# Kernel tuning notes

Hardware: AMD Instinct MI355X
Metric: run time of the kernel (lower is better)

The kernel has to match this reference:

```python
import jax, jax.numpy as jnp
import numpy as np

N_LAYERS = 4
NEG_SLOPE = 0.2  # GATv2 leaky_relu slope


def _segment_softmax(alpha, seg, num):
    # alpha: [E, H], seg: [E] target-node ids; every node has a self loop so no empty segments
    amax = jax.ops.segment_max(alpha, seg, num_segments=num)
    a = jnp.exp(alpha - amax[seg])
    denom = jax.ops.segment_sum(a, seg, num_segments=num)
    return a / denom[seg]


def _gat_block(x, relations, src, dst, rel_idx, Wl, bl, Wr, br, We, att, bias, Wb, bb):
    N, D = x.shape
    H = att.shape[0]
    C = att.shape[1]

    edge_attr = relations[rel_idx]  # [E, D]
    # add_self_loops with fill_value='mean': self-loop edge_attr = mean of incoming edge attrs
    deg = jax.ops.segment_sum(jnp.ones_like(dst, dtype=x.dtype), dst, num_segments=N)
    loop_attr = jax.ops.segment_sum(edge_attr, dst, num_segments=N) / jnp.maximum(deg, 1.0)[:, None]
    loops = jnp.arange(N, dtype=src.dtype)
    src_all = jnp.concatenate([src, loops])
    dst_all = jnp.concatenate([dst, loops])
    ea = jnp.concatenate([edge_attr, loop_attr], axis=0)  # [E+N, D]

    xl = (x @ Wl + bl).reshape(N, H, C)  # lin_l -> source transform
    xr = (x @ Wr + br).reshape(N, H, C)  # lin_r -> target transform
    eproj = (ea @ We).reshape(-1, H, C)  # lin_edge (no bias in PyG GATv2Conv)

    m = xl[src_all] + xr[dst_all] + eproj          # [E+N, H, C]
    m = jnp.where(m > 0, m, NEG_SLOPE * m)          # leaky_relu
    alpha = jnp.einsum('ehc,hc->eh', m, att)        # [E+N, H]
    alpha = _segment_softmax(alpha, dst_all, N)

    msg = xl[src_all] * alpha[..., None]            # [E+N, H, C]
    out = jax.ops.segment_sum(msg, dst_all, num_segments=N)  # [N, H, C]
    x_out = out.mean(axis=1) + bias                 # concat=False -> head mean, then bias

    # relation update: gnn.lin_edge -> relu -> block lin_edge
    r = jax.nn.relu(relations @ We)                 # [R, H*C]
    r_out = r @ Wb + bb                             # [R, D]
    return x_out, r_out


def setup_inputs() -> dict:
    key = jax.random.key(0)
    N, E, R, D, H = 10000, 40000, 2000, 128, 8
    L = N_LAYERS
    ks = jax.random.split(key, 16)
    s = 1.0 / np.sqrt(D)
    sb = 1.0 / np.sqrt(H * D)
    return {
        'x': jax.random.normal(ks[0], (N, D), dtype=jnp.float32),
        'edge_index': jax.random.randint(ks[1], (2, E), 0, N),
        'relations': jax.random.normal(ks[2], (R, D), dtype=jnp.float32),
        'relation_index': jax.random.randint(ks[3], (E,), 0, R),
        'Wl': jax.random.normal(ks[4], (L, D, H * D), dtype=jnp.float32) * s,
        'bl': jnp.zeros((L, H * D), dtype=jnp.float32),
        'Wr': jax.random.normal(ks[5], (L, D, H * D), dtype=jnp.float32) * s,
        'br': jnp.zeros((L, H * D), dtype=jnp.float32),
        'We': jax.random.normal(ks[6], (L, D, H * D), dtype=jnp.float32) * s,
        'att': jax.random.normal(ks[7], (L, H, D), dtype=jnp.float32) * s,
        'bias': jnp.zeros((L, D), dtype=jnp.float32),
        'Wb': jax.random.normal(ks[8], (L, H * D, D), dtype=jnp.float32) * sb,
        'bb': jnp.zeros((L, D), dtype=jnp.float32),
    }


def reference(x, edge_index, relations, relation_index, Wl, bl, Wr, br, We, att, bias, Wb, bb):
    src, dst = edge_index[0], edge_index[1]
    for l in range(N_LAYERS):
        x, relations = _gat_block(x, relations, src, dst, relation_index,
                                  Wl[l], bl[l], Wr[l], br[l], We[l], att[l],
                                  bias[l], Wb[l], bb[l])
    return (x, relations)
```

## Files before the change

kernel.cpp:

```cpp
#include <hip/hip_runtime.h>
#include <hip/hip_bf16.h>
#include <math.h>

#define NEG_SLOPE 0.2f
#define N_LAYERS 4

typedef __bf16 bf16_t;
typedef __attribute__((ext_vector_type(8))) __bf16 bf16x8;
typedef __attribute__((ext_vector_type(4))) __bf16 bf16x4;
typedef __attribute__((ext_vector_type(4))) float f32x4;
typedef __attribute__((ext_vector_type(8))) float f32x8;

static __device__ __forceinline__ float leaky(float v){ return v > 0.f ? v : NEG_SLOPE * v; }


__global__ void fill_int_kernel(int* __restrict__ p, int v, int n){
  int i = blockIdx.x*blockDim.x + threadIdx.x;
  if(i < n) p[i] = v;
}

__global__ void fill_bias_kernel(float* __restrict__ out, const float* __restrict__ b, int rows){
  int i = blockIdx.x*blockDim.x + threadIdx.x;
  if(i < rows * 128) out[i] = b[i & 127];
}

__global__ void hist_kernel(const int* __restrict__ dst, int E, int* __restrict__ deg){
  int e = blockIdx.x*blockDim.x + threadIdx.x;
  if(e < E) atomicAdd(&deg[dst[e]], 1);
}

__global__ void scan_kernel(const int* __restrict__ deg, int* __restrict__ offs, int N){
  __shared__ int wsum[4];
  int t = threadIdx.x, lane = t & 63, w = t >> 6;
  int carry = 0;
  for(int base = 0; base < N; base += 256){
    int v = (base + t < N) ? deg[base + t] : 0;
    int s = v;
#pragma unroll
    for(int o = 1; o < 64; o <<= 1){
      int u = __shfl_up(s, o);
      if(lane >= o) s += u;
    }
    if(lane == 63) wsum[w] = s;
    __syncthreads();
    int woff = 0;
    for(int i = 0; i < w; ++i) woff += wsum[i];
    if(base + t < N) offs[base + t + 1] = carry + woff + s;
    int tot = wsum[0] + wsum[1] + wsum[2] + wsum[3];
    __syncthreads();
    carry += tot;
  }
  if(t == 0) offs[0] = 0;
}

__global__ void scatter_kernel(const int* __restrict__ src, const int* __restrict__ dst,
                               const int* __restrict__ rel, int E,
                               const int* __restrict__ offs, int* __restrict__ cursor,
                               int* __restrict__ srcs, int* __restrict__ rels){
  int e = blockIdx.x*blockDim.x + threadIdx.x;
  if(e < E){
    int d = dst[e];
    int pos = offs[d] + atomicAdd(&cursor[d], 1);
    srcs[pos] = src[e];
    rels[pos] = rel[e];
  }
}


__global__ void deg_bhist_kernel(const int* __restrict__ offs, int N, int* __restrict__ blkhist){
  __shared__ int h[256];
  int t = threadIdx.x;
  h[t] = 0; __syncthreads();
  int i = blockIdx.x * 256 + t;
  if(i < N){
    int d = offs[i+1] - offs[i]; if(d > 255) d = 255;
    atomicAdd(&h[d], 1);
  }
  __syncthreads();
  blkhist[blockIdx.x * 256 + t] = h[t];
}

__global__ void deg_base_kernel(int* __restrict__ blkhist, int nb){
  __shared__ int tot[256];
  int d = threadIdx.x;
  int s = 0;
  for(int b = 0; b < nb; ++b){
    int v = blkhist[b * 256 + d];
    blkhist[b * 256 + d] = s;
    s += v;
  }
  tot[d] = s; __syncthreads();
  int start = 0;
  for(int k = d + 1; k < 256; ++k) start += tot[k];
  for(int b = 0; b < nb; ++b) blkhist[b * 256 + d] += start;
}

__global__ void deg_place_kernel(const int* __restrict__ offs, int N,
                                 const int* __restrict__ blkhist, int* __restrict__ order){
  __shared__ int cur[256];
  int t = threadIdx.x;
  cur[t] = blkhist[blockIdx.x * 256 + t];
  __syncthreads();
  int i = blockIdx.x * 256 + t;
  if(i < N){
    int d = offs[i+1] - offs[i]; if(d > 255) d = 255;
    int pos = atomicAdd(&cur[d], 1);
    order[pos] = i;
  }
}


__global__ void transpose_split_all_kernel(
    const float* __restrict__ Wl, const float* __restrict__ Wr,
    const float* __restrict__ We, const float* __restrict__ Wb,
    bf16_t* __restrict__ tWlh, bf16_t* __restrict__ tWll,
    bf16_t* __restrict__ tWrh, bf16_t* __restrict__ tWrl,
    bf16_t* __restrict__ tWeh, bf16_t* __restrict__ tWel,
    bf16_t* __restrict__ tWbh, bf16_t* __restrict__ tWbl){
  __shared__ float t[32][33];
  const int z = blockIdx.z, type = z >> 2, layer = z & 3;
  const int K  = (type < 3) ? 128 : 1024;
  const int Nn = (type < 3) ? 1024 : 128;
  const float* W; bf16_t* Th; bf16_t* Tl;
  if(type == 0){ W = Wl; Th = tWlh; Tl = tWll; }
  else if(type == 1){ W = Wr; Th = tWrh; Tl = tWrl; }
  else if(type == 2){ W = We; Th = tWeh; Tl = tWel; }
  else { W = Wb; Th = tWbh; Tl = tWbl; }
  size_t wo = (size_t)layer * 131072;
  W += wo; Th += wo; Tl += wo;
  const int nbx = K / 32;
  const int bx = blockIdx.x % nbx, by = blockIdx.x / nbx;
  const int k0 = bx * 32, n0 = by * 32;
  const int tx = threadIdx.x, ty = threadIdx.y;
#pragma unroll
  for(int i = 0; i < 4; ++i)
    t[ty*4 + i][tx] = W[(size_t)(k0 + ty*4 + i) * Nn + n0 + tx];
  __syncthreads();
#pragma unroll
  for(int i = 0; i < 4; ++i){
    int n = ty*4 + i;
    float v = t[tx][n];
    bf16_t h = (bf16_t)v;
    bf16_t l = (bf16_t)(v - (float)h);
    Th[(size_t)(n0 + n) * K + k0 + tx] = h;
    Tl[(size_t)(n0 + n) * K + k0 + tx] = l;
  }
}


template<bool RELU_A, bool HAS_BIAS, bool WRITE_BF16, bool SPLITK>
__global__ __launch_bounds__(256) void gemm_mfma_kernel(
    const float* __restrict__ A,
    const bf16_t* __restrict__ Bt_hi, const bf16_t* __restrict__ Bt_lo,
    const float* __restrict__ bias, float* __restrict__ C, bf16_t* __restrict__ Cb,
    int M, int N, int K){
  constexpr int LDK = 40;
  __shared__ bf16_t Ah[128 * LDK];
  __shared__ bf16_t Al[128 * LDK];
  __shared__ bf16_t Bh[128 * LDK];
  __shared__ bf16_t Bl[128 * LDK];

  const int tid  = threadIdx.x;
  const int lane = tid & 63;
  const int wid  = tid >> 6;
  const int wm = wid >> 1, wn = wid & 1;
  const int row0 = blockIdx.y * 128, col0 = blockIdx.x * 128;
  const int l15 = lane & 15;
  const int kb  = (lane >> 4) * 8;

  f32x4 acc[4][4];
#pragma unroll
  for(int m = 0; m < 4; ++m)
#pragma unroll
    for(int n = 0; n < 4; ++n) acc[m][n] = (f32x4){0.f, 0.f, 0.f, 0.f};

  int kbeg = 0, kend = K;
  if(SPLITK){ kbeg = blockIdx.z * 128; kend = kbeg + 128; }

  for(int k0 = kbeg; k0 < kend; k0 += 32){
    __syncthreads();
#pragma unroll
    for(int i = 0; i < 4; ++i){
      int f = tid + i * 256;
      int r = f >> 3, kq = f & 7;
      float4 v = make_float4(0.f, 0.f, 0.f, 0.f);
      if(row0 + r < M) v = *(const float4*)(A + (size_t)(row0 + r) * K + k0 + kq * 4);
      if(RELU_A){ v.x = fmaxf(v.x, 0.f); v.y = fmaxf(v.y, 0.f); v.z = fmaxf(v.z, 0.f); v.w = fmaxf(v.w, 0.f); }
      bf16_t h0 = (bf16_t)v.x, h1 = (bf16_t)v.y, h2 = (bf16_t)v.z, h3 = (bf16_t)v.w;
      bf16x4 hv = (bf16x4){h0, h1, h2, h3};
      bf16x4 lv = (bf16x4){(bf16_t)(v.x - (float)h0), (bf16_t)(v.y - (float)h1),
                           (bf16_t)(v.z - (float)h2), (bf16_t)(v.w - (float)h3)};
      *(bf16x4*)&Ah[r * LDK + kq * 4] = hv;
      *(bf16x4*)&Al[r * LDK + kq * 4] = lv;
    }
#pragma unroll
    for(int i = 0; i < 2; ++i){
      int f = tid + i * 256;
      int n = f >> 2, kq = f & 3;
      *(bf16x8*)&Bh[n * LDK + kq * 8] = *(const bf16x8*)(Bt_hi + (size_t)(col0 + n) * K + k0 + kq * 8);
      *(bf16x8*)&Bl[n * LDK + kq * 8] = *(const bf16x8*)(Bt_lo + (size_t)(col0 + n) * K + k0 + kq * 8);
    }
    __syncthreads();

    bf16x8 ah[4], al[4], bh[4], bl[4];
#pragma unroll
    for(int m = 0; m < 4; ++m){
      int r = wm * 64 + m * 16 + l15;
      ah[m] = *(bf16x8*)&Ah[r * LDK + kb];
      al[m] = *(bf16x8*)&Al[r * LDK + kb];
    }
#pragma unroll
    for(int n = 0; n < 4; ++n){
      int c = wn * 64 + n * 16 + l15;
      bh[n] = *(bf16x8*)&Bh[c * LDK + kb];
      bl[n] = *(bf16x8*)&Bl[c * LDK + kb];
    }
#pragma unroll
    for(int m = 0; m < 4; ++m)
#pragma unroll
      for(int n = 0; n < 4; ++n){
        acc[m][n] = __builtin_amdgcn_mfma_f32_16x16x32_bf16(ah[m], bh[n], acc[m][n], 0, 0, 0);
        acc[m][n] = __builtin_amdgcn_mfma_f32_16x16x32_bf16(ah[m], bl[n], acc[m][n], 0, 0, 0);
        acc[m][n] = __builtin_amdgcn_mfma_f32_16x16x32_bf16(al[m], bh[n], acc[m][n], 0, 0, 0);
      }
  }

#pragma unroll
  for(int n = 0; n < 4; ++n){
    int col = col0 + wn * 64 + n * 16 + l15;
    float bv = HAS_BIAS ? bias[col] : 0.f;
#pragma unroll
    for(int m = 0; m < 4; ++m){
      int rbase = row0 + wm * 64 + m * 16 + (lane >> 4) * 4;
#pragma unroll
      for(int r = 0; r < 4; ++r){
        if(rbase + r < M){
          size_t idx = (size_t)(rbase + r) * N + col;
          if(SPLITK){
            atomicAdd(&C[idx], acc[m][n][r]);
          } else {
            float val = acc[m][n][r] + bv;
            C[idx] = val;
            if(WRITE_BF16) Cb[idx] = (bf16_t)val;
          }
        }
      }
    }
  }
}


__global__ __launch_bounds__(256, 3) void gemm_proj_kernel(
    const float* __restrict__ Ar, const float* __restrict__ Ax,
    const bf16_t* __restrict__ Weh, const bf16_t* __restrict__ Wel,
    const bf16_t* __restrict__ Wlh, const bf16_t* __restrict__ Wll,
    const bf16_t* __restrict__ Wrh, const bf16_t* __restrict__ Wrl,
    const float* __restrict__ biasL, const float* __restrict__ biasR,
    float* __restrict__ rproj, bf16_t* __restrict__ rpb,
    bf16_t* __restrict__ xlb, bf16_t* __restrict__ xrb,
    int R, int Nn, int rjobs, int xjobs){
  constexpr int LDK = 40;
  __shared__ char smem[40960];
  bf16_t* Ah = (bf16_t*)smem;
  bf16_t* Al = (bf16_t*)(smem + 10240);
  bf16_t* Bh = (bf16_t*)(smem + 20480);
  bf16_t* Bl = (bf16_t*)(smem + 30720);

  const int tid  = threadIdx.x;
  const int lane = tid & 63;
  const int wid  = tid >> 6;
  const int wm = wid >> 1, wn = wid & 1;
  const int l15 = lane & 15;
  const int kb  = (lane >> 4) * 8;

  int nwg = gridDim.x;
  int lin = blockIdx.x;
  int w = ((nwg & 7) == 0) ? ((lin & 7) * (nwg >> 3) + (lin >> 3)) : lin;
  int job, jw;
  if(w < rjobs){ job = 0; jw = w; }
  else if(w < rjobs + xjobs){ job = 1; jw = w - rjobs; }
  else { job = 2; jw = w - rjobs - xjobs; }

  const float*  A   = (job == 0) ? Ar : Ax;
  const bf16_t* Bth = (job == 0) ? Weh : (job == 1) ? Wlh : Wrh;
  const bf16_t* Btl = (job == 0) ? Wel : (job == 1) ? Wll : Wrl;
  const int M = (job == 0) ? R : Nn;
  const int row0 = (jw >> 3) * 128, col0 = (jw & 7) * 128;

  f32x4 acc[4][4];
#pragma unroll
  for(int m = 0; m < 4; ++m)
#pragma unroll
    for(int n = 0; n < 4; ++n) acc[m][n] = (f32x4){0.f, 0.f, 0.f, 0.f};

  for(int k0 = 0; k0 < 128; k0 += 32){
    __syncthreads();
#pragma unroll
    for(int i = 0; i < 4; ++i){
      int f = tid + i * 256;
      int r = f >> 3, kq = f & 7;
      float4 v = make_float4(0.f, 0.f, 0.f, 0.f);
      if(row0 + r < M) v = *(const float4*)(A + (size_t)(row0 + r) * 128 + k0 + kq * 4);
      bf16_t h0 = (bf16_t)v.x, h1 = (bf16_t)v.y, h2 = (bf16_t)v.z, h3 = (bf16_t)v.w;
      bf16x4 hv = (bf16x4){h0, h1, h2, h3};
      bf16x4 lv = (bf16x4){(bf16_t)(v.x - (float)h0), (bf16_t)(v.y - (float)h1),
                           (bf16_t)(v.z - (float)h2), (bf16_t)(v.w - (float)h3)};
      *(bf16x4*)&Ah[r * LDK + kq * 4] = hv;
      *(bf16x4*)&Al[r * LDK + kq * 4] = lv;
    }
#pragma unroll
    for(int i = 0; i < 2; ++i){
      int f = tid + i * 256;
      int n = f >> 2, kq = f & 3;
      size_t g = (size_t)(col0 + n) * 128 + k0 + kq * 8;
      *(bf16x8*)&Bh[n * LDK + kq * 8] = *(const bf16x8*)(Bth + g);
      *(bf16x8*)&Bl[n * LDK + kq * 8] = *(const bf16x8*)(Btl + g);
    }
    __syncthreads();

    bf16x8 ah[4], al[4], bh[4], bl[4];
#pragma unroll
    for(int m = 0; m < 4; ++m){
      int r = wm * 64 + m * 16 + l15;
      ah[m] = *(bf16x8*)&Ah[r * LDK + kb];
      al[m] = *(bf16x8*)&Al[r * LDK + kb];
    }
#pragma unroll
    for(int n = 0; n < 4; ++n){
      int c = wn * 64 + n * 16 + l15;
      bh[n] = *(bf16x8*)&Bh[c * LDK + kb];
      bl[n] = *(bf16x8*)&Bl[c * LDK + kb];
    }
#pragma unroll
    for(int m = 0; m < 4; ++m)
#pragma unroll
      for(int n = 0; n < 4; ++n){
        acc[m][n] = __builtin_amdgcn_mfma_f32_16x16x32_bf16(ah[m], bh[n], acc[m][n], 0, 0, 0);
        acc[m][n] = __builtin_amdgcn_mfma_f32_16x16x32_bf16(ah[m], bl[n], acc[m][n], 0, 0, 0);
        acc[m][n] = __builtin_amdgcn_mfma_f32_16x16x32_bf16(al[m], bh[n], acc[m][n], 0, 0, 0);
      }
  }

  if(job == 0){
#pragma unroll
    for(int n = 0; n < 4; ++n){
      int col = col0 + wn * 64 + n * 16 + l15;
#pragma unroll
      for(int m = 0; m < 4; ++m){
        int rbase = row0 + wm * 64 + m * 16 + (lane >> 4) * 4;
#pragma unroll
        for(int r = 0; r < 4; ++r){
          if(rbase + r < M){
            size_t idx = (size_t)(rbase + r) * 1024 + col;
            float val = acc[m][n][r];
            rproj[idx] = val;
            rpb[idx]   = (bf16_t)val;
          }
        }
      }
    }
  } else {
    const float* bias = (job == 1) ? biasL : biasR;
    bf16_t* dst = (job == 1) ? xlb : xrb;
    bf16_t* tile = (bf16_t*)smem;
    __syncthreads();
#pragma unroll
    for(int n = 0; n < 4; ++n){
      int col = wn * 64 + n * 16 + l15;
      float bv = bias[col0 + col];
#pragma unroll
      for(int m = 0; m < 4; ++m){
        int rb = wm * 64 + m * 16 + (lane >> 4) * 4;
#pragma unroll
        for(int r = 0; r < 4; ++r)
          tile[(rb + r) * 132 + col] = (bf16_t)(acc[m][n][r] + bv);
      }
    }
    __syncthreads();
#pragma unroll
    for(int i = 0; i < 8; ++i){
      int ei = i * 2048 + tid * 8;
      int rr = ei >> 7, cc = ei & 127;
      if(row0 + rr < M)
        *(bf16x8*)(dst + (size_t)(row0 + rr) * 1024 + col0 + cc) = *(bf16x8*)&tile[rr * 132 + cc];
    }
  }
}


__global__ __launch_bounds__(256) void node_fused_kernel(
    const bf16_t* __restrict__ xlb, const bf16_t* __restrict__ xrb,
    const bf16_t* __restrict__ rpb,
    const int* __restrict__ offs, const int* __restrict__ srcs, const int* __restrict__ rels,
    const int* __restrict__ order,
    const float* __restrict__ att, const float* __restrict__ bias,
    float* __restrict__ xout, int N){
  __shared__ float tsh[2][128];
  const int wid  = threadIdx.x >> 6;
  const int lane = threadIdx.x & 63;
  const int nib  = wid >> 1;
  const int half = wid & 1;
  const int slot = blockIdx.x * 2 + nib;
  const bool active = slot < N;
  const int node = active ? order[slot] : 0;
  int beg = 0, end = 0;
  if(active){ beg = offs[node]; end = offs[node + 1]; }
  const float inv = 1.0f / fmaxf((float)(end - beg), 1.0f);

  const int o  = (half * 64 + lane) * 8;
  const int c0 = (lane & 15) * 8;
  const int h  = half * 4 + (lane >> 4);
  f32x8 av = *(const f32x8*)(att + h * 128 + c0);
  bf16x8 xrv = *(const bf16x8*)(xrb + (size_t)node * 1024 + o);
  f32x8 xr;
#pragma unroll
  for(int i = 0; i < 8; ++i) xr[i] = (float)xrv[i];

  f32x8 lac, num;
#pragma unroll
  for(int i = 0; i < 8; ++i){ lac[i] = 0.f; num[i] = 0.f; }
  float m = -INFINITY, den = 0.f;

  int p = beg;
  for(; p + 3 < end; p += 4){
    int s0 = srcs[p],   r0 = rels[p];
    int s1 = srcs[p+1], r1 = rels[p+1];
    int s2 = srcs[p+2], r2 = rels[p+2];
    int s3 = srcs[p+3], r3 = rels[p+3];
    bf16x8 a0 = *(const bf16x8*)(xlb + (size_t)s0 * 1024 + o);
    bf16x8 b0 = *(const bf16x8*)(rpb + (size_t)r0 * 1024 + o);
    bf16x8 a1 = *(const bf16x8*)(xlb + (size_t)s1 * 1024 + o);
    bf16x8 b1 = *(const bf16x8*)(rpb + (size_t)r1 * 1024 + o);
    bf16x8 a2 = *(const bf16x8*)(xlb + (size_t)s2 * 1024 + o);
    bf16x8 b2 = *(const bf16x8*)(rpb + (size_t)r2 * 1024 + o);
    bf16x8 a3 = *(const bf16x8*)(xlb + (size_t)s3 * 1024 + o);
    bf16x8 b3 = *(const bf16x8*)(rpb + (size_t)r3 * 1024 + o);
    float l0 = 0.f, l1 = 0.f, l2 = 0.f, l3 = 0.f;
#pragma unroll
    for(int i = 0; i < 8; ++i){
      float v;
      v = (float)b0[i]; lac[i] += v; l0 += leaky((float)a0[i] + xr[i] + v) * av[i];
      v = (float)b1[i]; lac[i] += v; l1 += leaky((float)a1[i] + xr[i] + v) * av[i];
      v = (float)b2[i]; lac[i] += v; l2 += leaky((float)a2[i] + xr[i] + v) * av[i];
      v = (float)b3[i]; lac[i] += v; l3 += leaky((float)a3[i] + xr[i] + v) * av[i];
    }
#pragma unroll
    for(int q = 8; q >= 1; q >>= 1){
      l0 += __shfl_xor(l0, q); l1 += __shfl_xor(l1, q);
      l2 += __shfl_xor(l2, q); l3 += __shfl_xor(l3, q);
    }
    float nm = fmaxf(m, fmaxf(fmaxf(l0, l1), fmaxf(l2, l3)));
    float sc = __expf(m - nm);
    float w0 = __expf(l0 - nm), w1 = __expf(l1 - nm);
    float w2 = __expf(l2 - nm), w3 = __expf(l3 - nm);
    den = den * sc + w0 + w1 + w2 + w3;
#pragma unroll
    for(int i = 0; i < 8; ++i)
      num[i] = num[i] * sc + w0 * (float)a0[i] + w1 * (float)a1[i]
                           + w2 * (float)a2[i] + w3 * (float)a3[i];
    m = nm;
  }
  for(; p < end; ++p){
    int s0 = srcs[p], r0 = rels[p];
    bf16x8 a0 = *(const bf16x8*)(xlb + (size_t)s0 * 1024 + o);
    bf16x8 b0 = *(const bf16x8*)(rpb + (size_t)r0 * 1024 + o);
    float l0 = 0.f;
#pragma unroll
    for(int i = 0; i < 8; ++i){
      float v = (float)b0[i]; lac[i] += v;
      l0 += leaky((float)a0[i] + xr[i] + v) * av[i];
    }
#pragma unroll
    for(int q = 8; q >= 1; q >>= 1) l0 += __shfl_xor(l0, q);
    float nm = fmaxf(m, l0);
    float sc = __expf(m - nm), w0 = __expf(l0 - nm);
    den = den * sc + w0;
#pragma unroll
    for(int i = 0; i < 8; ++i) num[i] = num[i] * sc + w0 * (float)a0[i];
    m = nm;
  }

  bf16x8 xlv = *(const bf16x8*)(xlb + (size_t)node * 1024 + o);
  float sl = 0.f;
#pragma unroll
  for(int i = 0; i < 8; ++i)
    sl += leaky((float)xlv[i] + xr[i] + lac[i] * inv) * av[i];
#pragma unroll
  for(int q = 8; q >= 1; q >>= 1) sl += __shfl_xor(sl, q);
  {
    float nm = fmaxf(m, sl);
    float sc = __expf(m - nm), w = __expf(sl - nm);
    den = den * sc + w;
#pragma unroll
    for(int i = 0; i < 8; ++i) num[i] = num[i] * sc + w * (float)xlv[i];
    m = nm;
  }

  f32x8 t;
  float d = 1.0f / den;
#pragma unroll
  for(int i = 0; i < 8; ++i) t[i] = num[i] * d;
#pragma unroll
  for(int i = 0; i < 8; ++i) t[i] += __shfl_xor(t[i], 16);
#pragma unroll
  for(int i = 0; i < 8; ++i) t[i] += __shfl_xor(t[i], 32);

  if(half == 1 && lane < 16){
#pragma unroll
    for(int i = 0; i < 8; ++i) tsh[nib][lane * 8 + i] = t[i];
  }
  __syncthreads();
  if(active && half == 0 && lane < 16){
    const float* bp = bias + lane * 8;
    float* op = xout + (size_t)node * 128 + lane * 8;
    float q[8];
#pragma unroll
    for(int i = 0; i < 8; ++i) q[i] = (t[i] + tsh[nib][lane * 8 + i]) * 0.125f + bp[i];
    *(float4*)op       = make_float4(q[0], q[1], q[2], q[3]);
    *(float4*)(op + 4) = make_float4(q[4], q[5], q[6], q[7]);
  }
}


extern "C" void kernel_launch(void* const* d_in, const int* in_sizes, int n_in,
                              void* d_out, int out_size, void* d_ws, size_t ws_size,
                              hipStream_t stream){
  const float* x0   = (const float*)d_in[0];
  const int*   ei   = (const int*)d_in[1];
  const float* rel0 = (const float*)d_in[2];
  const int*   ridx = (const int*)d_in[3];
  const float* Wl   = (const float*)d_in[4];
  const float* bl   = (const float*)d_in[5];
  const float* Wr   = (const float*)d_in[6];
  const float* br   = (const float*)d_in[7];
  const float* We   = (const float*)d_in[8];
  const float* att  = (const float*)d_in[9];
  const float* bias = (const float*)d_in[10];
  const float* Wb   = (const float*)d_in[11];
  const float* bb   = (const float*)d_in[12];

  const int D = 128, HC = 1024;
  const int N = in_sizes[0] / D;
  const int E = in_sizes[1] / 2;
  const int R = in_sizes[2] / D;
  const int WSZ = D * HC;
  const int NB = (N + 255) / 256;

  const int* src = ei;
  const int* dst = ei + E;

  char* ws = (char*)d_ws;
  size_t off = 0;
  auto alloc = [&](size_t bytes) -> void* {
    void* p = ws + off;
    off += (bytes + 255) & ~(size_t)255;
    return p;
  };
  float*  rproj  = (float*)alloc((size_t)R * HC * 4);
  bf16_t* xlb    = (bf16_t*)alloc((size_t)N * HC * 2);
  bf16_t* xrb    = (bf16_t*)alloc((size_t)N * HC * 2);
  bf16_t* rpb    = (bf16_t*)alloc((size_t)R * HC * 2);
  float*  xbufA  = (float*)alloc((size_t)N * D * 4);
  float*  xbufB  = (float*)alloc((size_t)N * D * 4);
  float*  rbufA  = (float*)alloc((size_t)R * D * 4);
  float*  rbufB  = (float*)alloc((size_t)R * D * 4);
  int* zbase   = (int*)alloc((size_t)(2 * N) * 4);
  int* deg     = zbase;
  int* cursor  = zbase + N;
  int* offs    = (int*)alloc((size_t)(N + 1) * 4);
  int* blkhist = (int*)alloc((size_t)NB * 256 * 4);
  int* order   = (int*)alloc((size_t)N * 4);
  int* srcs    = (int*)alloc((size_t)E * 4);
  int* rels    = (int*)alloc((size_t)E * 4);
  bf16_t* tWl_h = (bf16_t*)alloc((size_t)N_LAYERS * WSZ * 2);
  bf16_t* tWl_l = (bf16_t*)alloc((size_t)N_LAYERS * WSZ * 2);
  bf16_t* tWr_h = (bf16_t*)alloc((size_t)N_LAYERS * WSZ * 2);
  bf16_t* tWr_l = (bf16_t*)alloc((size_t)N_LAYERS * WSZ * 2);
  bf16_t* tWe_h = (bf16_t*)alloc((size_t)N_LAYERS * WSZ * 2);
  bf16_t* tWe_l = (bf16_t*)alloc((size_t)N_LAYERS * WSZ * 2);
  bf16_t* tWb_h = (bf16_t*)alloc((size_t)N_LAYERS * WSZ * 2);
  bf16_t* tWb_l = (bf16_t*)alloc((size_t)N_LAYERS * WSZ * 2);
  float* xbuf[2] = {xbufA, xbufB};
  float* rbuf[2] = {rbufA, rbufB};

  float* out_x = (float*)d_out;
  float* out_r = (float*)d_out + (size_t)N * D;

  fill_int_kernel<<<(2 * N + 255) / 256, 256, 0, stream>>>(zbase, 0, 2 * N);
  hist_kernel<<<(E + 255) / 256, 256, 0, stream>>>(dst, E, deg);
  scan_kernel<<<1, 256, 0, stream>>>(deg, offs, N);
  scatter_kernel<<<(E + 255) / 256, 256, 0, stream>>>(src, dst, ridx, E, offs, cursor, srcs, rels);
  deg_bhist_kernel<<<NB, 256, 0, stream>>>(offs, N, blkhist);
  deg_base_kernel<<<1, 256, 0, stream>>>(blkhist, NB);
  deg_place_kernel<<<NB, 256, 0, stream>>>(offs, N, blkhist, order);

  transpose_split_all_kernel<<<dim3(128, 1, 16), dim3(32, 8), 0, stream>>>(
      Wl, Wr, We, Wb, tWl_h, tWl_l, tWr_h, tWr_l, tWe_h, tWe_l, tWb_h, tWb_l);

  const int rjobs = ((R + 127) / 128) * (HC / 128);
  const int xjobs = ((N + 127) / 128) * (HC / 128);

  for(int l = 0; l < N_LAYERS; ++l){
    const float* xin = (l == 0) ? x0   : xbuf[(l + 1) & 1];
    float*       xo  = (l == N_LAYERS - 1) ? out_x : xbuf[l & 1];
    const float* rin = (l == 0) ? rel0 : rbuf[(l + 1) & 1];
    float*       ro  = (l == N_LAYERS - 1) ? out_r : rbuf[l & 1];
    size_t wo = (size_t)l * WSZ;
    const float* bl_l  = bl + (size_t)l * HC;
    const float* br_l  = br + (size_t)l * HC;
    const float* att_l = att + (size_t)l * 8 * 128;
    const float* bias_l= bias + (size_t)l * D;
    const float* bb_l  = bb + (size_t)l * D;

    gemm_proj_kernel<<<rjobs + 2 * xjobs, 256, 0, stream>>>(
        rin, xin, tWe_h + wo, tWe_l + wo, tWl_h + wo, tWl_l + wo, tWr_h + wo, tWr_l + wo,
        bl_l, br_l, rproj, rpb, xlb, xrb, R, N, rjobs, xjobs);
    node_fused_kernel<<<(2 * N + 3) / 4, 256, 0, stream>>>(
        xlb, xrb, rpb, offs, srcs, rels, order, att_l, bias_l, xo, N);
    fill_bias_kernel<<<(R * 128 + 255) / 256, 256, 0, stream>>>(ro, bb_l, R);
    gemm_mfma_kernel<true,false,false,true><<<dim3(D/128, (R+127)/128, 8), 256, 0, stream>>>(
        rproj, tWb_h + wo, tWb_l + wo, nullptr, ro, nullptr, R, D, HC);
  }
}
```

Baseline: 443.3 us.

## Fuse bias fill and relu split into projection GEMM, pipeline B loads, add relation GEMM

The projection GEMM gains a fourth job type that writes the relation bias fill, replacing a separate fill kernel. It now also emits the ReLU'd relation projection pre-split into bf16 hi/lo arrays, so the new split-K relation GEMM reads bf16 instead of fp32. B tiles are double-buffered through registers, and A fragments are loaded straight from global memory into registers instead of being staged in LDS. The node kernel's tail loop is folded into a masked 4-wide loop. The trade-offs are more global traffic for A and more atomic adds from the 16-way split-K, and the fill job must finish before the atomics land, which relies on stream ordering.

```diff
diff --git a/kernel.cpp b/kernel.cpp
--- a/kernel.cpp
+++ b/kernel.cpp
@@ -17,11 +17,6 @@
 __global__ void fill_int_kernel(int* __restrict__ p, int v, int n){
   int i = blockIdx.x*blockDim.x + threadIdx.x;
   if(i < n) p[i] = v;
-}
-
-__global__ void fill_bias_kernel(float* __restrict__ out, const float* __restrict__ b, int rows){
-  int i = blockIdx.x*blockDim.x + threadIdx.x;
-  if(i < rows * 128) out[i] = b[i & 127];
 }
 
 __global__ void hist_kernel(const int* __restrict__ dst, int E, int* __restrict__ deg){
@@ -148,123 +143,18 @@
 }
 
 
-template<bool RELU_A, bool HAS_BIAS, bool WRITE_BF16, bool SPLITK>
-__global__ __launch_bounds__(256) void gemm_mfma_kernel(
-    const float* __restrict__ A,
-    const bf16_t* __restrict__ Bt_hi, const bf16_t* __restrict__ Bt_lo,
-    const float* __restrict__ bias, float* __restrict__ C, bf16_t* __restrict__ Cb,
-    int M, int N, int K){
-  constexpr int LDK = 40;
-  __shared__ bf16_t Ah[128 * LDK];
-  __shared__ bf16_t Al[128 * LDK];
-  __shared__ bf16_t Bh[128 * LDK];
-  __shared__ bf16_t Bl[128 * LDK];
-
-  const int tid  = threadIdx.x;
-  const int lane = tid & 63;
-  const int wid  = tid >> 6;
-  const int wm = wid >> 1, wn = wid & 1;
-  const int row0 = blockIdx.y * 128, col0 = blockIdx.x * 128;
-  const int l15 = lane & 15;
-  const int kb  = (lane >> 4) * 8;
-
-  f32x4 acc[4][4];
-#pragma unroll
-  for(int m = 0; m < 4; ++m)
-#pragma unroll
-    for(int n = 0; n < 4; ++n) acc[m][n] = (f32x4){0.f, 0.f, 0.f, 0.f};
-
-  int kbeg = 0, kend = K;
-  if(SPLITK){ kbeg = blockIdx.z * 128; kend = kbeg + 128; }
-
-  for(int k0 = kbeg; k0 < kend; k0 += 32){
-    __syncthreads();
-#pragma unroll
-    for(int i = 0; i < 4; ++i){
-      int f = tid + i * 256;
-      int r = f >> 3, kq = f & 7;
-      float4 v = make_float4(0.f, 0.f, 0.f, 0.f);
-      if(row0 + r < M) v = *(const float4*)(A + (size_t)(row0 + r) * K + k0 + kq * 4);
-      if(RELU_A){ v.x = fmaxf(v.x, 0.f); v.y = fmaxf(v.y, 0.f); v.z = fmaxf(v.z, 0.f); v.w = fmaxf(v.w, 0.f); }
-      bf16_t h0 = (bf16_t)v.x, h1 = (bf16_t)v.y, h2 = (bf16_t)v.z, h3 = (bf16_t)v.w;
-      bf16x4 hv = (bf16x4){h0, h1, h2, h3};
-      bf16x4 lv = (bf16x4){(bf16_t)(v.x - (float)h0), (bf16_t)(v.y - (float)h1),
-                           (bf16_t)(v.z - (float)h2), (bf16_t)(v.w - (float)h3)};
-      *(bf16x4*)&Ah[r * LDK + kq * 4] = hv;
-      *(bf16x4*)&Al[r * LDK + kq * 4] = lv;
-    }
-#pragma unroll
-    for(int i = 0; i < 2; ++i){
-      int f = tid + i * 256;
-      int n = f >> 2, kq = f & 3;
-      *(bf16x8*)&Bh[n * LDK + kq * 8] = *(const bf16x8*)(Bt_hi + (size_t)(col0 + n) * K + k0 + kq * 8);
-      *(bf16x8*)&Bl[n * LDK + kq * 8] = *(const bf16x8*)(Bt_lo + (size_t)(col0 + n) * K + k0 + kq * 8);
-    }
-    __syncthreads();
-
-    bf16x8 ah[4], al[4], bh[4], bl[4];
-#pragma unroll
-    for(int m = 0; m < 4; ++m){
-      int r = wm * 64 + m * 16 + l15;
-      ah[m] = *(bf16x8*)&Ah[r * LDK + kb];
-      al[m] = *(bf16x8*)&Al[r * LDK + kb];
-    }
-#pragma unroll
-    for(int n = 0; n < 4; ++n){
-      int c = wn * 64 + n * 16 + l15;
-      bh[n] = *(bf16x8*)&Bh[c * LDK + kb];
-      bl[n] = *(bf16x8*)&Bl[c * LDK + kb];
-    }
-#pragma unroll
-    for(int m = 0; m < 4; ++m)
-#pragma unroll
-      for(int n = 0; n < 4; ++n){
-        acc[m][n] = __builtin_amdgcn_mfma_f32_16x16x32_bf16(ah[m], bh[n], acc[m][n], 0, 0, 0);
-        acc[m][n] = __builtin_amdgcn_mfma_f32_16x16x32_bf16(ah[m], bl[n], acc[m][n], 0, 0, 0);
-        acc[m][n] = __builtin_amdgcn_mfma_f32_16x16x32_bf16(al[m], bh[n], acc[m][n], 0, 0, 0);
-      }
-  }
-
-#pragma unroll
-  for(int n = 0; n < 4; ++n){
-    int col = col0 + wn * 64 + n * 16 + l15;
-    float bv = HAS_BIAS ? bias[col] : 0.f;
-#pragma unroll
-    for(int m = 0; m < 4; ++m){
-      int rbase = row0 + wm * 64 + m * 16 + (lane >> 4) * 4;
-#pragma unroll
-      for(int r = 0; r < 4; ++r){
-        if(rbase + r < M){
-          size_t idx = (size_t)(rbase + r) * N + col;
-          if(SPLITK){
-            atomicAdd(&C[idx], acc[m][n][r]);
-          } else {
-            float val = acc[m][n][r] + bv;
-            C[idx] = val;
-            if(WRITE_BF16) Cb[idx] = (bf16_t)val;
-          }
-        }
-      }
-    }
-  }
-}
-
-
-__global__ __launch_bounds__(256, 3) void gemm_proj_kernel(
+__global__ __launch_bounds__(256) void gemm_proj_kernel(
     const float* __restrict__ Ar, const float* __restrict__ Ax,
     const bf16_t* __restrict__ Weh, const bf16_t* __restrict__ Wel,
     const bf16_t* __restrict__ Wlh, const bf16_t* __restrict__ Wll,
     const bf16_t* __restrict__ Wrh, const bf16_t* __restrict__ Wrl,
     const float* __restrict__ biasL, const float* __restrict__ biasR,
-    float* __restrict__ rproj, bf16_t* __restrict__ rpb,
+    const float* __restrict__ biasB, float* __restrict__ ro,
+    bf16_t* __restrict__ rpb, bf16_t* __restrict__ rph, bf16_t* __restrict__ rpl,
     bf16_t* __restrict__ xlb, bf16_t* __restrict__ xrb,
-    int R, int Nn, int rjobs, int xjobs){
+    int R, int Nn, int rjobs, int xjobs, int bjobs){
   constexpr int LDK = 40;
   __shared__ char smem[40960];
-  bf16_t* Ah = (bf16_t*)smem;
-  bf16_t* Al = (bf16_t*)(smem + 10240);
-  bf16_t* Bh = (bf16_t*)(smem + 20480);
-  bf16_t* Bl = (bf16_t*)(smem + 30720);
 
   const int tid  = threadIdx.x;
   const int lane = tid & 63;
@@ -279,7 +169,18 @@
   int job, jw;
   if(w < rjobs){ job = 0; jw = w; }
   else if(w < rjobs + xjobs){ job = 1; jw = w - rjobs; }
-  else { job = 2; jw = w - rjobs - xjobs; }
+  else if(w < rjobs + 2 * xjobs){ job = 2; jw = w - rjobs - xjobs; }
+  else { job = 3; jw = w - rjobs - 2 * xjobs; }
+
+  if(job == 3){
+    int idx8 = (jw * 256 + tid) * 8;
+    if(idx8 < R * 128){
+      const float* bp = biasB + (idx8 & 127);
+      *(float4*)(ro + idx8)     = *(const float4*)bp;
+      *(float4*)(ro + idx8 + 4) = *(const float4*)(bp + 4);
+    }
+    return;
+  }
 
   const float*  A   = (job == 0) ? Ar : Ax;
   const bf16_t* Bth = (job == 0) ? Weh : (job == 1) ? Wlh : Wrh;
@@ -287,49 +188,67 @@
   const int M = (job == 0) ? R : Nn;
   const int row0 = (jw >> 3) * 128, col0 = (jw & 7) * 128;
 
+  const int f0 = tid, f1 = tid + 256;
+  const int ns0 = f0 >> 2, kq0 = f0 & 3;
+  const int ns1 = f1 >> 2, kq1 = f1 & 3;
+  const size_t gb0 = (size_t)(col0 + ns0) * 128 + kq0 * 8;
+  const size_t gb1 = (size_t)(col0 + ns1) * 128 + kq1 * 8;
+  const int lo0 = ns0 * LDK + kq0 * 8;
+  const int lo1 = ns1 * LDK + kq1 * 8;
+
+  bf16x8 sbh0 = *(const bf16x8*)(Bth + gb0);
+  bf16x8 sbl0 = *(const bf16x8*)(Btl + gb0);
+  bf16x8 sbh1 = *(const bf16x8*)(Bth + gb1);
+  bf16x8 sbl1 = *(const bf16x8*)(Btl + gb1);
+  {
+    bf16_t* bhB = (bf16_t*)smem;
+    bf16_t* blB = (bf16_t*)(smem + 10240);
+    *(bf16x8*)&bhB[lo0] = sbh0; *(bf16x8*)&blB[lo0] = sbl0;
+    *(bf16x8*)&bhB[lo1] = sbh1; *(bf16x8*)&blB[lo1] = sbl1;
+  }
+
   f32x4 acc[4][4];
 #pragma unroll
   for(int m = 0; m < 4; ++m)
 #pragma unroll
     for(int n = 0; n < 4; ++n) acc[m][n] = (f32x4){0.f, 0.f, 0.f, 0.f};
 
-  for(int k0 = 0; k0 < 128; k0 += 32){
+#pragma unroll
+  for(int t = 0; t < 4; ++t){
     __syncthreads();
-#pragma unroll
-    for(int i = 0; i < 4; ++i){
-      int f = tid + i * 256;
-      int r = f >> 3, kq = f & 7;
-      float4 v = make_float4(0.f, 0.f, 0.f, 0.f);
-      if(row0 + r < M) v = *(const float4*)(A + (size_t)(row0 + r) * 128 + k0 + kq * 4);
-      bf16_t h0 = (bf16_t)v.x, h1 = (bf16_t)v.y, h2 = (bf16_t)v.z, h3 = (bf16_t)v.w;
-      bf16x4 hv = (bf16x4){h0, h1, h2, h3};
-      bf16x4 lv = (bf16x4){(bf16_t)(v.x - (float)h0), (bf16_t)(v.y - (float)h1),
-                           (bf16_t)(v.z - (float)h2), (bf16_t)(v.w - (float)h3)};
-      *(bf16x4*)&Ah[r * LDK + kq * 4] = hv;
-      *(bf16x4*)&Al[r * LDK + kq * 4] = lv;
-    }
-#pragma unroll
-    for(int i = 0; i < 2; ++i){
-      int f = tid + i * 256;
-      int n = f >> 2, kq = f & 3;
-      size_t g = (size_t)(col0 + n) * 128 + k0 + kq * 8;
-      *(bf16x8*)&Bh[n * LDK + kq * 8] = *(const bf16x8*)(Bth + g);
-      *(bf16x8*)&Bl[n * LDK + kq * 8] = *(const bf16x8*)(Btl + g);
-    }
-    __syncthreads();
-
-    bf16x8 ah[4], al[4], bh[4], bl[4];
+    const int k0 = t * 32;
+    if(t < 3){
+      sbh0 = *(const bf16x8*)(Bth + gb0 + k0 + 32);
+      sbl0 = *(const bf16x8*)(Btl + gb0 + k0 + 32);
+      sbh1 = *(const bf16x8*)(Bth + gb1 + k0 + 32);
+      sbl1 = *(const bf16x8*)(Btl + gb1 + k0 + 32);
+    }
+    bf16x8 ah[4], al[4];
 #pragma unroll
     for(int m = 0; m < 4; ++m){
-      int r = wm * 64 + m * 16 + l15;
-      ah[m] = *(bf16x8*)&Ah[r * LDK + kb];
-      al[m] = *(bf16x8*)&Al[r * LDK + kb];
-    }
+      int row = row0 + wm * 64 + m * 16 + l15;
+      float4 v0 = make_float4(0.f,0.f,0.f,0.f), v1 = make_float4(0.f,0.f,0.f,0.f);
+      if(row < M){
+        const float* ap = A + (size_t)row * 128 + k0 + kb;
+        v0 = *(const float4*)ap;
+        v1 = *(const float4*)(ap + 4);
+      }
+      bf16_t h0 = (bf16_t)v0.x, h1 = (bf16_t)v0.y, h2 = (bf16_t)v0.z, h3 = (bf16_t)v0.w;
+      bf16_t h4 = (bf16_t)v1.x, h5 = (bf16_t)v1.y, h6 = (bf16_t)v1.z, h7 = (bf16_t)v1.w;
+      ah[m] = (bf16x8){h0,h1,h2,h3,h4,h5,h6,h7};
+      al[m] = (bf16x8){(bf16_t)(v0.x-(float)h0), (bf16_t)(v0.y-(float)h1),
+                       (bf16_t)(v0.z-(float)h2), (bf16_t)(v0.w-(float)h3),
+                       (bf16_t)(v1.x-(float)h4), (bf16_t)(v1.y-(float)h5),
+                       (bf16_t)(v1.z-(float)h6), (bf16_t)(v1.w-(float)h7)};
+    }
+    bf16_t* bhB = (bf16_t*)(smem + (t & 1) * 20480);
+    bf16_t* blB = (bf16_t*)(smem + (t & 1) * 20480 + 10240);
+    bf16x8 bh[4], bl[4];
 #pragma unroll
     for(int n = 0; n < 4; ++n){
       int c = wn * 64 + n * 16 + l15;
-      bh[n] = *(bf16x8*)&Bh[c * LDK + kb];
-      bl[n] = *(bf16x8*)&Bl[c * LDK + kb];
+      bh[n] = *(bf16x8*)&bhB[c * LDK + kb];
+      bl[n] = *(bf16x8*)&blB[c * LDK + kb];
     }
 #pragma unroll
     for(int m = 0; m < 4; ++m)
@@ -339,6 +258,12 @@
         acc[m][n] = __builtin_amdgcn_mfma_f32_16x16x32_bf16(ah[m], bl[n], acc[m][n], 0, 0, 0);
         acc[m][n] = __builtin_amdgcn_mfma_f32_16x16x32_bf16(al[m], bh[n], acc[m][n], 0, 0, 0);
       }
+    if(t < 3){
+      bf16_t* bhN = (bf16_t*)(smem + ((t + 1) & 1) * 20480);
+      bf16_t* blN = (bf16_t*)(smem + ((t + 1) & 1) * 20480 + 10240);
+      *(bf16x8*)&bhN[lo0] = sbh0; *(bf16x8*)&blN[lo0] = sbl0;
+      *(bf16x8*)&bhN[lo1] = sbh1; *(bf16x8*)&blN[lo1] = sbl1;
+    }
   }
 
   if(job == 0){
@@ -352,9 +277,12 @@
         for(int r = 0; r < 4; ++r){
           if(rbase + r < M){
             size_t idx = (size_t)(rbase + r) * 1024 + col;
-            float val = acc[m][n][r];
-            rproj[idx] = val;
-            rpb[idx]   = (bf16_t)val;
+            float v = acc[m][n][r];
+            rpb[idx] = (bf16_t)v;
+            float vr = fmaxf(v, 0.f);
+            bf16_t h = (bf16_t)vr;
+            rph[idx] = h;
+            rpl[idx] = (bf16_t)(vr - (float)h);
           }
         }
       }
@@ -383,6 +311,94 @@
       int rr = ei >> 7, cc = ei & 127;
       if(row0 + rr < M)
         *(bf16x8*)(dst + (size_t)(row0 + rr) * 1024 + col0 + cc) = *(bf16x8*)&tile[rr * 132 + cc];
+    }
+  }
+}
+
+
+__global__ __launch_bounds__(256) void gemm_rel_kernel(
+    const bf16_t* __restrict__ Agh, const bf16_t* __restrict__ Agl,
+    const bf16_t* __restrict__ Bth, const bf16_t* __restrict__ Btl,
+    float* __restrict__ C, int M){
+  constexpr int LDK = 40;
+  __shared__ bf16_t Ah[128 * LDK];
+  __shared__ bf16_t Al[128 * LDK];
+  __shared__ bf16_t Bh[128 * LDK];
+  __shared__ bf16_t Bl[128 * LDK];
+
+  const int tid  = threadIdx.x;
+  const int lane = tid & 63;
+  const int wid  = tid >> 6;
+  const int wm = wid >> 1, wn = wid & 1;
+  const int row0 = blockIdx.y * 128;
+  const int l15 = lane & 15;
+  const int kb  = (lane >> 4) * 8;
+  const int kbeg = blockIdx.z * 64;
+
+  f32x4 acc[4][4];
+#pragma unroll
+  for(int m = 0; m < 4; ++m)
+#pragma unroll
+    for(int n = 0; n < 4; ++n) acc[m][n] = (f32x4){0.f, 0.f, 0.f, 0.f};
+
+#pragma unroll
+  for(int tt = 0; tt < 2; ++tt){
+    int k0 = kbeg + tt * 32;
+    __syncthreads();
+#pragma unroll
+    for(int i = 0; i < 2; ++i){
+      int f = tid + i * 256;
+      int r = f >> 2, kq = f & 3;
+      bf16x8 vh = {}, vl = {};
+      if(row0 + r < M){
+        size_t g = (size_t)(row0 + r) * 1024 + k0 + kq * 8;
+        vh = *(const bf16x8*)(Agh + g);
+        vl = *(const bf16x8*)(Agl + g);
+      }
+      *(bf16x8*)&Ah[r * LDK + kq * 8] = vh;
+      *(bf16x8*)&Al[r * LDK + kq * 8] = vl;
+      size_t gb = (size_t)r * 1024 + k0 + kq * 8;
+      *(bf16x8*)&Bh[r * LDK + kq * 8] = *(const bf16x8*)(Bth + gb);
+      *(bf16x8*)&Bl[r * LDK + kq * 8] = *(const bf16x8*)(Btl + gb);
+    }
+    __syncthreads();
+
+    bf16x8 ah[4], al[4], bh[4], bl[4];
+#pragma unroll
+    for(int m = 0; m < 4; ++m){
+      int r = wm * 64 + m * 16 + l15;
+      ah[m] = *(bf16x8*)&Ah[r * LDK + kb];
+      al[m] = *(bf16x8*)&Al[r * LDK + kb];
+    }
+#pragma unroll
+    for(int n = 0; n < 4; ++n){
+      int c = wn * 64 + n * 16 + l15;
+      bh[n] = *(bf16x8*)&Bh[c * LDK + kb];
+      bl[n] = *(bf16x8*)&Bl[c * LDK + kb];
+    }
+#pragma unroll
+    for(int m = 0; m < 4; ++m)
+#pragma unroll
+      for(int n = 0; n < 4; ++n){
+        acc[m][n] = __builtin_amdgcn_mfma_f32_16x16x32_bf16(ah[m], bh[n], acc[m][n], 0, 0, 0);
+        acc[m][n] = __builtin_amdgcn_mfma_f32_16x16x32_bf16(ah[m], bl[n], acc[m][n], 0, 0, 0);
+        acc[m][n] = __builtin_amdgcn_mfma_f32_16x16x32_bf16(al[m], bh[n], acc[m][n], 0, 0, 0);
+      }
+  }
+
+#pragma unroll
+  for(int n = 0; n < 4; ++n){
+    int col = wn * 64 + n * 16 + l15;
+    if(col < 128){
+#pragma unroll
+      for(int m = 0; m < 4; ++m){
+        int rbase = row0 + wm * 64 + m * 16 + (lane >> 4) * 4;
+#pragma unroll
+        for(int r = 0; r < 4; ++r){
+          if(rbase + r < M)
+            atomicAdd(&C[(size_t)(rbase + r) * 128 + col], acc[m][n][r]);
+        }
+      }
     }
   }
 }
@@ -421,12 +437,18 @@
   for(int i = 0; i < 8; ++i){ lac[i] = 0.f; num[i] = 0.f; }
   float m = -INFINITY, den = 0.f;
 
-  int p = beg;
-  for(; p + 3 < end; p += 4){
-    int s0 = srcs[p],   r0 = rels[p];
-    int s1 = srcs[p+1], r1 = rels[p+1];
-    int s2 = srcs[p+2], r2 = rels[p+2];
-    int s3 = srcs[p+3], r3 = rels[p+3];
+  for(int p = beg; p < end; p += 4){
+    int rem = end - p;
+    int i1 = (rem > 1) ? p + 1 : p;
+    int i2 = (rem > 2) ? p + 2 : p;
+    int i3 = (rem > 3) ? p + 3 : p;
+    float k1 = (rem > 1) ? 1.f : 0.f;
+    float k2 = (rem > 2) ? 1.f : 0.f;
+    float k3 = (rem > 3) ? 1.f : 0.f;
+    int s0 = srcs[p],  r0 = rels[p];
+    int s1 = srcs[i1], r1 = rels[i1];
+    int s2 = srcs[i2], r2 = rels[i2];
+    int s3 = srcs[i3], r3 = rels[i3];
     bf16x8 a0 = *(const bf16x8*)(xlb + (size_t)s0 * 1024 + o);
     bf16x8 b0 = *(const bf16x8*)(rpb + (size_t)r0 * 1024 + o);
     bf16x8 a1 = *(const bf16x8*)(xlb + (size_t)s1 * 1024 + o);
@@ -438,17 +460,21 @@
     float l0 = 0.f, l1 = 0.f, l2 = 0.f, l3 = 0.f;
 #pragma unroll
     for(int i = 0; i < 8; ++i){
-      float v;
-      v = (float)b0[i]; lac[i] += v; l0 += leaky((float)a0[i] + xr[i] + v) * av[i];
-      v = (float)b1[i]; lac[i] += v; l1 += leaky((float)a1[i] + xr[i] + v) * av[i];
-      v = (float)b2[i]; lac[i] += v; l2 += leaky((float)a2[i] + xr[i] + v) * av[i];
-      v = (float)b3[i]; lac[i] += v; l3 += leaky((float)a3[i] + xr[i] + v) * av[i];
+      float v0 = (float)b0[i], v1 = (float)b1[i], v2 = (float)b2[i], v3 = (float)b3[i];
+      lac[i] += v0 + k1 * v1 + k2 * v2 + k3 * v3;
+      l0 += leaky((float)a0[i] + xr[i] + v0) * av[i];
+      l1 += leaky((float)a1[i] + xr[i] + v1) * av[i];
+      l2 += leaky((float)a2[i] + xr[i] + v2) * av[i];
+      l3 += leaky((float)a3[i] + xr[i] + v3) * av[i];
     }
 #pragma unroll
     for(int q = 8; q >= 1; q >>= 1){
       l0 += __shfl_xor(l0, q); l1 += __shfl_xor(l1, q);
       l2 += __shfl_xor(l2, q); l3 += __shfl_xor(l3, q);
     }
+    l1 = (k1 > 0.f) ? l1 : -INFINITY;
+    l2 = (k2 > 0.f) ? l2 : -INFINITY;
+    l3 = (k3 > 0.f) ? l3 : -INFINITY;
     float nm = fmaxf(m, fmaxf(fmaxf(l0, l1), fmaxf(l2, l3)));
     float sc = __expf(m - nm);
     float w0 = __expf(l0 - nm), w1 = __expf(l1 - nm);
@@ -460,25 +486,6 @@
                            + w2 * (float)a2[i] + w3 * (float)a3[i];
     m = nm;
   }
-  for(; p < end; ++p){
-    int s0 = srcs[p], r0 = rels[p];
-    bf16x8 a0 = *(const bf16x8*)(xlb + (size_t)s0 * 1024 + o);
-    bf16x8 b0 = *(const bf16x8*)(rpb + (size_t)r0 * 1024 + o);
-    float l0 = 0.f;
-#pragma unroll
-    for(int i = 0; i < 8; ++i){
-      float v = (float)b0[i]; lac[i] += v;
-      l0 += leaky((float)a0[i] + xr[i] + v) * av[i];
-    }
-#pragma unroll
-    for(int q = 8; q >= 1; q >>= 1) l0 += __shfl_xor(l0, q);
-    float nm = fmaxf(m, l0);
-    float sc = __expf(m - nm), w0 = __expf(l0 - nm);
-    den = den * sc + w0;
-#pragma unroll
-    for(int i = 0; i < 8; ++i) num[i] = num[i] * sc + w0 * (float)a0[i];
-    m = nm;
-  }
 
   bf16x8 xlv = *(const bf16x8*)(xlb + (size_t)node * 1024 + o);
   float sl = 0.f;
@@ -489,10 +496,10 @@
   for(int q = 8; q >= 1; q >>= 1) sl += __shfl_xor(sl, q);
   {
     float nm = fmaxf(m, sl);
-    float sc = __expf(m - nm), w = __expf(sl - nm);
-    den = den * sc + w;
-#pragma unroll
-    for(int i = 0; i < 8; ++i) num[i] = num[i] * sc + w * (float)xlv[i];
+    float sc = __expf(m - nm), wv = __expf(sl - nm);
+    den = den * sc + wv;
+#pragma unroll
+    for(int i = 0; i < 8; ++i) num[i] = num[i] * sc + wv * (float)xlv[i];
     m = nm;
   }
 
@@ -556,10 +563,11 @@
     off += (bytes + 255) & ~(size_t)255;
     return p;
   };
-  float*  rproj  = (float*)alloc((size_t)R * HC * 4);
   bf16_t* xlb    = (bf16_t*)alloc((size_t)N * HC * 2);
   bf16_t* xrb    = (bf16_t*)alloc((size_t)N * HC * 2);
   bf16_t* rpb    = (bf16_t*)alloc((size_t)R * HC * 2);
+  bf16_t* rph    = (bf16_t*)alloc((size_t)R * HC * 2);
+  bf16_t* rpl    = (bf16_t*)alloc((size_t)R * HC * 2);
   float*  xbufA  = (float*)alloc((size_t)N * D * 4);
   float*  xbufB  = (float*)alloc((size_t)N * D * 4);
   float*  rbufA  = (float*)alloc((size_t)R * D * 4);
@@ -599,6 +607,8 @@
 
   const int rjobs = ((R + 127) / 128) * (HC / 128);
   const int xjobs = ((N + 127) / 128) * (HC / 128);
+  const int bjobs = 128;
+  const int nwg = rjobs + 2 * xjobs + bjobs;
 
   for(int l = 0; l < N_LAYERS; ++l){
     const float* xin = (l == 0) ? x0   : xbuf[(l + 1) & 1];
@@ -612,13 +622,12 @@
     const float* bias_l= bias + (size_t)l * D;
     const float* bb_l  = bb + (size_t)l * D;
 
-    gemm_proj_kernel<<<rjobs + 2 * xjobs, 256, 0, stream>>>(
+    gemm_proj_kernel<<<nwg, 256, 0, stream>>>(
         rin, xin, tWe_h + wo, tWe_l + wo, tWl_h + wo, tWl_l + wo, tWr_h + wo, tWr_l + wo,
-        bl_l, br_l, rproj, rpb, xlb, xrb, R, N, rjobs, xjobs);
+        bl_l, br_l, bb_l, ro, rpb, rph, rpl, xlb, xrb, R, N, rjobs, xjobs, bjobs);
     node_fused_kernel<<<(2 * N + 3) / 4, 256, 0, stream>>>(
         xlb, xrb, rpb, offs, srcs, rels, order, att_l, bias_l, xo, N);
-    fill_bias_kernel<<<(R * 128 + 255) / 256, 256, 0, stream>>>(ro, bb_l, R);
-    gemm_mfma_kernel<true,false,false,true><<<dim3(D/128, (R+127)/128, 8), 256, 0, stream>>>(
-        rproj, tWb_h + wo, tWb_l + wo, nullptr, ro, nullptr, R, D, HC);
-  }
-}
+    gemm_rel_kernel<<<dim3(1, (R + 127) / 128, 16), 256, 0, stream>>>(
+        rph, rpl, tWb_h + wo, tWb_l + wo, ro, R);
+  }
+}
```

Result: slower. 509.3 us (+14.9%).
